# Performance work log

Hardware: AMD Instinct MI355X
Metric: run time of the kernel (lower is better)

The kernel has to match this reference:

```python
import jax, jax.numpy as jnp
import numpy as np

SIZE = 64            # size
DIST = 4             # distance (4x4x4 unshared window)
PAD = DIST // 2      # 2
DS = SIZE - 4        # depth of voxel grid (60)
CONVEY = 0.9
RATE = 5
FC_IN = DS * SIZE * SIZE  # (size-4)*size*size = 245760


def setup_inputs() -> dict:
    key = jax.random.key(0)
    ks = jax.random.split(key, 8)
    vinput = jax.random.normal(ks[0], (DS, SIZE, SIZE, 4), dtype=jnp.float32)
    # location-specific (unshared) 4x4x4 synapse weights per voxel
    synapse = jax.random.normal(ks[1], (DS, SIZE, SIZE, DIST, DIST, DIST), dtype=jnp.float32)
    W1 = jax.random.normal(ks[2], (1024, FC_IN), dtype=jnp.float32) / np.float32(np.sqrt(FC_IN))
    b1 = jnp.zeros((1024,), jnp.float32)
    W2 = jax.random.normal(ks[3], (128, 1024), dtype=jnp.float32) / np.float32(np.sqrt(1024))
    b2 = jnp.zeros((128,), jnp.float32)
    W3 = jax.random.normal(ks[4], (10, 128), dtype=jnp.float32) / np.float32(np.sqrt(128))
    b3 = jnp.zeros((10,), jnp.float32)
    return {"vinput": vinput, "synapse": synapse, "W1": W1, "b1": b1,
            "W2": W2, "b2": b2, "W3": W3, "b3": b3}


def _forward(vinput, synapse, W1, b1, W2, b2, W3, b3):
    # frame is zeros, so neuron_matrix = pad(vinput) on the 3 spatial dims
    nm = jnp.pad(vinput, ((PAD, PAD), (PAD, PAD), (PAD, PAD), (0, 0)))  # (DS+2P, S+2P, S+2P, 4)
    ofs = jnp.arange(DIST)
    # gather indices for the 4x4x4 windows anchored at the top-left (as in the source)
    wi = (jnp.arange(DS)[:, None] + ofs)[:, None, None, :, None, None]
    wj = (jnp.arange(SIZE)[:, None] + ofs)[None, :, None, None, :, None]
    wk = (jnp.arange(SIZE)[:, None] + ofs)[None, None, :, None, None, :]
    for _ in range(RATE):
        # synapse (d,d,d) broadcasts over channel, so the full sum factors
        # through the channel-sum of the neuron matrix.
        ns = nm.sum(-1)                       # (DS+2P, S+2P, S+2P)
        win = ns[wi, wj, wk]                  # (DS, S, S, d, d, d)
        core = jnp.einsum('ijkabc,ijkabc->ijk', synapse, win)  # (DS, S, S)
        # dummy is written only at [0:DS, 0:S, 0:S]; border stays zero.
        nm = jnp.zeros_like(nm).at[:DS, :SIZE, :SIZE, :].set(
            (jax.nn.relu(core) * CONVEY)[..., None])
    x = nm[PAD:DS + PAD, PAD:SIZE + PAD, PAD:SIZE + PAD, :]  # (DS, S, S, 4)
    x = x.reshape(-1, FC_IN)                                 # (4, FC_IN), row-major like torch view
    x = jax.nn.relu(x @ W1.T + b1)
    x = jax.nn.relu(x @ W2.T + b2)
    return x @ W3.T + b3                                     # (4, 10)


def reference(vinput, synapse, W1, b1, W2, b2, W3, b3):
    return _forward(vinput, synapse, W1, b1, W2, b2, W3, b3)
```

## Files before the change

kernel.cpp:

```cpp
#include <hip/hip_runtime.h>

#define DSX 60
#define SZ  64
#define NPT (DSX*SZ*SZ)
#define NS_P 64
#define NS_Q 68
#define NS_R 68
#define NS_SZ (NS_P*NS_Q*NS_R)
#define P_PER_ROW 61440
#define KSPLIT 8
#define P_CHUNK (P_PER_ROW / KSPLIT)
#define PB_SLAB (15*NS_Q*NS_R)
#define NS_BLOCKS 1156
#define TR_BLOCKS (NPT / 64)
#define PT_BLOCKS (NPT / 256)
#define PF_BLOCKS 512
#define PF_ITERS  16

typedef float fx4 __attribute__((ext_vector_type(4)));

__device__ __forceinline__ unsigned rne_bf16(float x) {
    unsigned b = __float_as_uint(x);
    return (b + 0x7fffu + ((b >> 16) & 1u)) >> 16;
}

__global__ __launch_bounds__(256) void prologue(const float* __restrict__ vin,
                                                const float* __restrict__ syn,
                                                float* __restrict__ PB0,
                                                float* __restrict__ PB1,
                                                uint2* __restrict__ synP) {
    if (blockIdx.x < NS_BLOCKS) {
        int t = blockIdx.x * 256 + threadIdx.x;
        if (t >= NS_SZ) return;
        int r = t % NS_R;
        int q = (t / NS_R) % NS_Q;
        int p = t / (NS_R * NS_Q);
        float val = 0.f;
        if (p >= 2 && p < 62 && q >= 2 && q < 66 && r >= 2 && r < 66) {
            const float* b = vin + ((((size_t)(p - 2) * SZ) + (q - 2)) * SZ + (r - 2)) * 4;
            val = (b[0] + b[1]) + (b[2] + b[3]);
        }
        PB0[t] = val;
        PB1[t] = 0.f;
    } else {
        __shared__ float tile[64 * 65];
        int t0 = (blockIdx.x - NS_BLOCKS) * 64;
        const fx4* s4 = (const fx4*)syn;
#pragma unroll
        for (int r = 0; r < 4; r++) {
            int idx = r * 256 + threadIdx.x;
            int pl = idx >> 4, g = idx & 15;
            fx4 v = s4[(size_t)(t0 + pl) * 16 + g];
            int base = pl * 65 + g * 4;
            tile[base] = v.x; tile[base + 1] = v.y; tile[base + 2] = v.z; tile[base + 3] = v.w;
        }
        __syncthreads();
        int l = threadIdx.x & 63;
        int wv = threadIdx.x >> 6;
#pragma unroll
        for (int r = 0; r < 4; r++) {
            int g = r * 4 + wv;
            int base = l * 65 + g * 4;
            uint2 u;
            u.x = rne_bf16(tile[base])     | (rne_bf16(tile[base + 1]) << 16);
            u.y = rne_bf16(tile[base + 2]) | (rne_bf16(tile[base + 3]) << 16);
            synP[(size_t)g * NPT + t0 + l] = u;
        }
    }
}

__global__ __launch_bounds__(256) void conv_kernel(const float* __restrict__ PBin,
                                                   const uint2* __restrict__ synP,
                                                   float* __restrict__ PBout,
                                                   const float* __restrict__ W1,
                                                   float* __restrict__ pfdump,
                                                   int slice) {
    if (blockIdx.x < PT_BLOCKS) {
        int t = blockIdx.x * 256 + threadIdx.x;
        int k = t & 63;
        int j = (t >> 6) & 63;
        int i = t >> 12;
        float acc = 0.f;
#pragma unroll
        for (int g = 0; g < 16; g++) {
            uint2 u = synP[(size_t)g * NPT + t];
            float w0 = __uint_as_float(u.x << 16);
            float w1 = __uint_as_float(u.x & 0xffff0000u);
            float w2 = __uint_as_float(u.y << 16);
            float w3 = __uint_as_float(u.y & 0xffff0000u);
            int a = g >> 2, b = g & 3;
            const float* nrow = PBin + ((size_t)(i + a) * NS_Q + (j + b)) * NS_R + k;
            acc += w0 * nrow[0] + w1 * nrow[1] + w2 * nrow[2] + w3 * nrow[3];
        }
        PBout[((size_t)i * NS_Q + j) * NS_R + k] = acc > 0.f ? acc * 3.6f : 0.f;
    } else {
        int b = blockIdx.x - PT_BLOCKS;
        const fx4* w = (const fx4*)W1 +
            (size_t)slice * (PF_BLOCKS * 256 * PF_ITERS) +
            (size_t)b * (256 * PF_ITERS) + threadIdx.x;
        float acc = 0.f;
#pragma unroll
        for (int it = 0; it < PF_ITERS; it++) {
            fx4 v = w[it * 256];
            acc += (v.x + v.y) + (v.z + v.w);
        }
        if (acc == 1234.56789f) pfdump[b] = acc;
    }
}

__global__ __launch_bounds__(256) void gemv1(const float* __restrict__ W1,
                                             const float* __restrict__ PB,
                                             float* __restrict__ partial) {
    int n = blockIdx.x >> 3;
    int c = blockIdx.x & 7;
    const fx4* w4 = (const fx4*)(W1 + (size_t)n * (P_PER_ROW * 4));
    float a0 = 0.f, a1 = 0.f, a2 = 0.f, a3 = 0.f;
#pragma unroll 5
    for (int it = 0; it < 15; it++) {
        int p1 = c * P_CHUNK + it * 256 + threadIdx.x;
        int p2 = p1 + 15 * 256;
        fx4 wa = w4[p1];
        fx4 wb = w4[p2];
        float sa = (wa.x + wa.y) + (wa.z + wa.w);
        float sb = (wb.x + wb.y) + (wb.z + wb.w);
        int i1 = p1 >> 12, j1 = (p1 >> 6) & 63, k1 = p1 & 63;
        int i2 = p2 >> 12, j2 = (p2 >> 6) & 63, k2 = p2 & 63;
        int base1 = ((i1 + 2) * NS_Q + (j1 + 2)) * NS_R + (k1 + 2);
        int base2 = ((i2 + 2) * NS_Q + (j2 + 2)) * NS_R + (k2 + 2);
        a0 += sa * PB[base1] + sb * PB[base2];
        a1 += sa * PB[base1 + PB_SLAB] + sb * PB[base2 + PB_SLAB];
        a2 += sa * PB[base1 + 2 * PB_SLAB] + sb * PB[base2 + 2 * PB_SLAB];
        a3 += sa * PB[base1 + 3 * PB_SLAB] + sb * PB[base2 + 3 * PB_SLAB];
    }
#pragma unroll
    for (int off = 32; off; off >>= 1) {
        a0 += __shfl_down(a0, off);
        a1 += __shfl_down(a1, off);
        a2 += __shfl_down(a2, off);
        a3 += __shfl_down(a3, off);
    }
    __shared__ float red[4][4];
    int lane = threadIdx.x & 63, wv = threadIdx.x >> 6;
    if (lane == 0) { red[wv][0] = a0; red[wv][1] = a1; red[wv][2] = a2; red[wv][3] = a3; }
    __syncthreads();
    if (threadIdx.x < 4) {
        int r = threadIdx.x;
        float s = (red[0][r] + red[1][r]) + (red[2][r] + red[3][r]);
        partial[((size_t)c * 4 + r) * 1024 + n] = s;
    }
}

__global__ __launch_bounds__(256) void fc2(const float* __restrict__ W2,
                                           const float* __restrict__ b1,
                                           const float* __restrict__ b2,
                                           const float* __restrict__ partial,
                                           float* __restrict__ h2) {
    int n = blockIdx.x;
    float a0 = 0.f, a1 = 0.f, a2 = 0.f, a3 = 0.f;
    for (int e = threadIdx.x; e < 1024; e += 256) {
        float w = W2[(size_t)n * 1024 + e];
        float be = b1[e];
#pragma unroll
        for (int r = 0; r < 4; r++) {
            float acc = 0.f;
#pragma unroll
            for (int cc = 0; cc < KSPLIT; cc++) acc += partial[(cc * 4 + r) * 1024 + e];
            float h = 0.25f * acc + be;
            h = h > 0.f ? h : 0.f;
            if (r == 0) a0 += w * h;
            else if (r == 1) a1 += w * h;
            else if (r == 2) a2 += w * h;
            else a3 += w * h;
        }
    }
#pragma unroll
    for (int off = 32; off; off >>= 1) {
        a0 += __shfl_down(a0, off);
        a1 += __shfl_down(a1, off);
        a2 += __shfl_down(a2, off);
        a3 += __shfl_down(a3, off);
    }
    __shared__ float red[4][4];
    int lane = threadIdx.x & 63, wv = threadIdx.x >> 6;
    if (lane == 0) { red[wv][0] = a0; red[wv][1] = a1; red[wv][2] = a2; red[wv][3] = a3; }
    __syncthreads();
    if (threadIdx.x < 4) {
        int r = threadIdx.x;
        float s = (red[0][r] + red[1][r]) + (red[2][r] + red[3][r]) + b2[n];
        h2[(size_t)r * 128 + n] = s > 0.f ? s : 0.f;
    }
}

__global__ __launch_bounds__(64) void fc3(const float* __restrict__ W3,
                                          const float* __restrict__ b3,
                                          const float* __restrict__ h2,
                                          float* __restrict__ out) {
    int t = threadIdx.x;
    if (t < 40) {
        int r = t / 10, n = t % 10;
        float a = b3[n];
        for (int e = 0; e < 128; e++) a += W3[(size_t)n * 128 + e] * h2[(size_t)r * 128 + e];
        out[t] = a;
    }
}

extern "C" void kernel_launch(void* const* d_in, const int* in_sizes, int n_in,
                              void* d_out, int out_size, void* d_ws, size_t ws_size,
                              hipStream_t stream) {
    const float* vin = (const float*)d_in[0];
    const float* syn = (const float*)d_in[1];
    const float* W1  = (const float*)d_in[2];
    const float* b1  = (const float*)d_in[3];
    const float* W2  = (const float*)d_in[4];
    const float* b2  = (const float*)d_in[5];
    const float* W3  = (const float*)d_in[6];
    const float* b3  = (const float*)d_in[7];
    float* out = (float*)d_out;

    float* ws = (float*)d_ws;
    float* PB0 = ws;
    float* PB1 = PB0 + NS_SZ;
    float* partial = PB1 + NS_SZ;
    float* h2 = partial + 32 * 1024;
    float* pfdump = h2 + 1024;
    uint2* synP = (uint2*)(pfdump + 1024);

    prologue<<<NS_BLOCKS + TR_BLOCKS, 256, 0, stream>>>(vin, syn, PB0, PB1, synP);
    float* cur = PB0; float* nxt = PB1;
    for (int it = 0; it < 5; it++) {
        conv_kernel<<<PT_BLOCKS + PF_BLOCKS, 256, 0, stream>>>(cur, synP, nxt, W1, pfdump, it);
        float* tmp = cur; cur = nxt; nxt = tmp;
    }
    gemv1<<<1024 * KSPLIT, 256, 0, stream>>>(W1, cur, partial);
    fc2<<<128, 256, 0, stream>>>(W2, b1, b2, partial, h2);
    fc3<<<1, 64, 0, stream>>>(W3, b3, h2, out);
}
```

Before: 263.2 us.

## Drop W1 L2 prefetch, use nontemporal W1 loads, fuse fc2 and fc3

Removes the extra blocks in the conv kernel that streamed slices of W1 to warm the cache ahead of the big GEMV. gemv1 now reads W1 with nontemporal loads, which are meant to stream without polluting the cache. fc2 and fc3 are merged into one single-block kernel that keeps h1 and h2 in shared memory, saving a launch and a global round trip. In exchange, W1 is no longer prefetched while the conv runs, so the GEMV may read all of it from HBM. The single-block fc2 also serialises 1024-long dot products per thread with strided W2 reads.

Result: slower. 298.7 us (+13.5%).

```diff
diff --git a/kernel.cpp b/kernel.cpp
--- a/kernel.cpp
+++ b/kernel.cpp
@@ -14,8 +14,6 @@
 #define NS_BLOCKS 1156
 #define TR_BLOCKS (NPT / 64)
 #define PT_BLOCKS (NPT / 256)
-#define PF_BLOCKS 512
-#define PF_ITERS  16
 
 typedef float fx4 __attribute__((ext_vector_type(4)));
 
@@ -71,41 +69,24 @@
 
 __global__ __launch_bounds__(256) void conv_kernel(const float* __restrict__ PBin,
                                                    const uint2* __restrict__ synP,
-                                                   float* __restrict__ PBout,
-                                                   const float* __restrict__ W1,
-                                                   float* __restrict__ pfdump,
-                                                   int slice) {
-    if (blockIdx.x < PT_BLOCKS) {
-        int t = blockIdx.x * 256 + threadIdx.x;
-        int k = t & 63;
-        int j = (t >> 6) & 63;
-        int i = t >> 12;
-        float acc = 0.f;
-#pragma unroll
-        for (int g = 0; g < 16; g++) {
-            uint2 u = synP[(size_t)g * NPT + t];
-            float w0 = __uint_as_float(u.x << 16);
-            float w1 = __uint_as_float(u.x & 0xffff0000u);
-            float w2 = __uint_as_float(u.y << 16);
-            float w3 = __uint_as_float(u.y & 0xffff0000u);
-            int a = g >> 2, b = g & 3;
-            const float* nrow = PBin + ((size_t)(i + a) * NS_Q + (j + b)) * NS_R + k;
-            acc += w0 * nrow[0] + w1 * nrow[1] + w2 * nrow[2] + w3 * nrow[3];
-        }
-        PBout[((size_t)i * NS_Q + j) * NS_R + k] = acc > 0.f ? acc * 3.6f : 0.f;
-    } else {
-        int b = blockIdx.x - PT_BLOCKS;
-        const fx4* w = (const fx4*)W1 +
-            (size_t)slice * (PF_BLOCKS * 256 * PF_ITERS) +
-            (size_t)b * (256 * PF_ITERS) + threadIdx.x;
-        float acc = 0.f;
-#pragma unroll
-        for (int it = 0; it < PF_ITERS; it++) {
-            fx4 v = w[it * 256];
-            acc += (v.x + v.y) + (v.z + v.w);
-        }
-        if (acc == 1234.56789f) pfdump[b] = acc;
-    }
+                                                   float* __restrict__ PBout) {
+    int t = blockIdx.x * 256 + threadIdx.x;
+    int k = t & 63;
+    int j = (t >> 6) & 63;
+    int i = t >> 12;
+    float acc = 0.f;
+#pragma unroll
+    for (int g = 0; g < 16; g++) {
+        uint2 u = synP[(size_t)g * NPT + t];
+        float w0 = __uint_as_float(u.x << 16);
+        float w1 = __uint_as_float(u.x & 0xffff0000u);
+        float w2 = __uint_as_float(u.y << 16);
+        float w3 = __uint_as_float(u.y & 0xffff0000u);
+        int a = g >> 2, b = g & 3;
+        const float* nrow = PBin + ((size_t)(i + a) * NS_Q + (j + b)) * NS_R + k;
+        acc += w0 * nrow[0] + w1 * nrow[1] + w2 * nrow[2] + w3 * nrow[3];
+    }
+    PBout[((size_t)i * NS_Q + j) * NS_R + k] = acc > 0.f ? acc * 3.6f : 0.f;
 }
 
 __global__ __launch_bounds__(256) void gemv1(const float* __restrict__ W1,
@@ -119,8 +100,8 @@
     for (int it = 0; it < 15; it++) {
         int p1 = c * P_CHUNK + it * 256 + threadIdx.x;
         int p2 = p1 + 15 * 256;
-        fx4 wa = w4[p1];
-        fx4 wb = w4[p2];
+        fx4 wa = __builtin_nontemporal_load(&w4[p1]);
+        fx4 wb = __builtin_nontemporal_load(&w4[p2]);
         float sa = (wa.x + wa.y) + (wa.z + wa.w);
         float sb = (wb.x + wb.y) + (wb.z + wb.w);
         int i1 = p1 >> 12, j1 = (p1 >> 6) & 63, k1 = p1 & 63;
@@ -150,57 +131,43 @@
     }
 }
 
-__global__ __launch_bounds__(256) void fc2(const float* __restrict__ W2,
-                                           const float* __restrict__ b1,
-                                           const float* __restrict__ b2,
-                                           const float* __restrict__ partial,
-                                           float* __restrict__ h2) {
-    int n = blockIdx.x;
-    float a0 = 0.f, a1 = 0.f, a2 = 0.f, a3 = 0.f;
-    for (int e = threadIdx.x; e < 1024; e += 256) {
-        float w = W2[(size_t)n * 1024 + e];
-        float be = b1[e];
-#pragma unroll
-        for (int r = 0; r < 4; r++) {
-            float acc = 0.f;
-#pragma unroll
-            for (int cc = 0; cc < KSPLIT; cc++) acc += partial[(cc * 4 + r) * 1024 + e];
-            float h = 0.25f * acc + be;
-            h = h > 0.f ? h : 0.f;
-            if (r == 0) a0 += w * h;
-            else if (r == 1) a1 += w * h;
-            else if (r == 2) a2 += w * h;
-            else a3 += w * h;
-        }
-    }
-#pragma unroll
-    for (int off = 32; off; off >>= 1) {
-        a0 += __shfl_down(a0, off);
-        a1 += __shfl_down(a1, off);
-        a2 += __shfl_down(a2, off);
-        a3 += __shfl_down(a3, off);
-    }
-    __shared__ float red[4][4];
-    int lane = threadIdx.x & 63, wv = threadIdx.x >> 6;
-    if (lane == 0) { red[wv][0] = a0; red[wv][1] = a1; red[wv][2] = a2; red[wv][3] = a3; }
+__global__ __launch_bounds__(256) void fc23(const float* __restrict__ W2,
+                                            const float* __restrict__ b1,
+                                            const float* __restrict__ b2,
+                                            const float* __restrict__ W3,
+                                            const float* __restrict__ b3,
+                                            const float* __restrict__ partial,
+                                            float* __restrict__ out) {
+    __shared__ float h1s[4][1024];
+    __shared__ float h2s[4][128];
+    for (int idx = threadIdx.x; idx < 4096; idx += 256) {
+        int r = idx >> 10, e = idx & 1023;
+        float acc = 0.f;
+#pragma unroll
+        for (int cc = 0; cc < KSPLIT; cc++) acc += partial[(cc * 4 + r) * 1024 + e];
+        float h = 0.25f * acc + b1[e];
+        h1s[r][e] = h > 0.f ? h : 0.f;
+    }
     __syncthreads();
-    if (threadIdx.x < 4) {
-        int r = threadIdx.x;
-        float s = (red[0][r] + red[1][r]) + (red[2][r] + red[3][r]) + b2[n];
-        h2[(size_t)r * 128 + n] = s > 0.f ? s : 0.f;
-    }
-}
-
-__global__ __launch_bounds__(64) void fc3(const float* __restrict__ W3,
-                                          const float* __restrict__ b3,
-                                          const float* __restrict__ h2,
-                                          float* __restrict__ out) {
-    int t = threadIdx.x;
-    if (t < 40) {
-        int r = t / 10, n = t % 10;
+    for (int idx = threadIdx.x; idx < 512; idx += 256) {
+        int r = idx >> 7, n = idx & 127;
+        const float* w = W2 + (size_t)n * 1024;
+        float c0 = 0.f, c1 = 0.f, c2 = 0.f, c3 = 0.f;
+        for (int e = 0; e < 1024; e += 4) {
+            c0 += w[e] * h1s[r][e];
+            c1 += w[e + 1] * h1s[r][e + 1];
+            c2 += w[e + 2] * h1s[r][e + 2];
+            c3 += w[e + 3] * h1s[r][e + 3];
+        }
+        float acc = ((c0 + c1) + (c2 + c3)) + b2[n];
+        h2s[r][n] = acc > 0.f ? acc : 0.f;
+    }
+    __syncthreads();
+    if (threadIdx.x < 40) {
+        int r = threadIdx.x / 10, n = threadIdx.x % 10;
         float a = b3[n];
-        for (int e = 0; e < 128; e++) a += W3[(size_t)n * 128 + e] * h2[(size_t)r * 128 + e];
-        out[t] = a;
+        for (int e = 0; e < 128; e++) a += W3[(size_t)n * 128 + e] * h2s[r][e];
+        out[threadIdx.x] = a;
     }
 }
 
@@ -221,17 +188,14 @@
     float* PB0 = ws;
     float* PB1 = PB0 + NS_SZ;
     float* partial = PB1 + NS_SZ;
-    float* h2 = partial + 32 * 1024;
-    float* pfdump = h2 + 1024;
-    uint2* synP = (uint2*)(pfdump + 1024);
+    uint2* synP = (uint2*)(partial + 32 * 1024);
 
     prologue<<<NS_BLOCKS + TR_BLOCKS, 256, 0, stream>>>(vin, syn, PB0, PB1, synP);
     float* cur = PB0; float* nxt = PB1;
     for (int it = 0; it < 5; it++) {
-        conv_kernel<<<PT_BLOCKS + PF_BLOCKS, 256, 0, stream>>>(cur, synP, nxt, W1, pfdump, it);
+        conv_kernel<<<PT_BLOCKS, 256, 0, stream>>>(cur, synP, nxt);
         float* tmp = cur; cur = nxt; nxt = tmp;
     }
     gemv1<<<1024 * KSPLIT, 256, 0, stream>>>(W1, cur, partial);
-    fc2<<<128, 256, 0, stream>>>(W2, b1, b2, partial, h2);
-    fc3<<<1, 64, 0, stream>>>(W3, b3, h2, out);
-}
+    fc23<<<1, 256, 0, stream>>>(W2, b1, b2, W3, b3, partial, out);
+}
```
